# Performance work log

Measured on AMD Instinct MI355X. Metric: run time of the kernel, lower is better.

## Reference

```python
import jax, jax.numpy as jnp
import numpy as np

SOLVER_STEPS = 10
POINT_DIM = 2
CONTEXT_DIM = 128
HIDDEN_DIM = 256


def setup_inputs() -> dict:
    key = jax.random.key(0)
    ks = jax.random.split(key, 8)
    B, N = 64, 4096
    in_dim = POINT_DIM + 1 + CONTEXT_DIM  # 131
    std = 0.1  # torch nn.init.normal_(std=0.1)
    x = jax.random.normal(ks[0], (B, N, POINT_DIM), jnp.float32)
    context = jax.random.normal(ks[1], (B, CONTEXT_DIM), jnp.float32)
    w1 = std * jax.random.normal(ks[2], (in_dim, HIDDEN_DIM), jnp.float32)
    w2 = std * jax.random.normal(ks[3], (HIDDEN_DIM, HIDDEN_DIM), jnp.float32)
    w3 = std * jax.random.normal(ks[4], (HIDDEN_DIM, HIDDEN_DIM), jnp.float32)
    w4 = std * 0.1 * jax.random.normal(ks[5], (HIDDEN_DIM, POINT_DIM), jnp.float32)  # last layer weight * 0.1
    b1 = jnp.zeros((HIDDEN_DIM,), jnp.float32)
    b2 = jnp.zeros((HIDDEN_DIM,), jnp.float32)
    b3 = jnp.zeros((HIDDEN_DIM,), jnp.float32)
    b4 = jnp.zeros((POINT_DIM,), jnp.float32)
    return {"x": x, "context": context, "w1": w1, "b1": b1, "w2": w2, "b2": b2,
            "w3": w3, "b3": b3, "w4": w4, "b4": b4}


def _mlp(pts, t, ctx, w1, b1, w2, b2, w3, b3, w4, b4):
    # pts: [B,N,2], ctx: [B,N,C] -> velocity [B,N,2]
    B, N, _ = pts.shape
    t_vec = jnp.full((B, N, 1), t, dtype=pts.dtype)
    h = jnp.concatenate([pts, t_vec, ctx], axis=-1)
    h = jax.nn.silu(h @ w1 + b1)  # Swish == silu
    h = jax.nn.silu(h @ w2 + b2)
    h = jax.nn.silu(h @ w3 + b3)
    return h @ w4 + b4


def reference(x, context, w1, b1, w2, b2, w3, b3, w4, b4):
    B, N, D = x.shape
    ctx = jnp.broadcast_to(context[:, None, :], (B, N, context.shape[-1]))
    dt = jnp.asarray(1.0 / SOLVER_STEPS, x.dtype)
    ts = jnp.linspace(0.0, 1.0, SOLVER_STEPS + 1, dtype=x.dtype)[:SOLVER_STEPS]
    e0 = jnp.broadcast_to(jnp.array([1.0, 0.0], x.dtype), x.shape)
    e1 = jnp.broadcast_to(jnp.array([0.0, 1.0], x.dtype), x.shape)

    def step(carry, t_i):
        pts, log_det = carry
        f = lambda p: _mlp(p, t_i, ctx, w1, b1, w2, b2, w3, b3, w4, b4)
        # exact divergence = trace of per-point 2x2 Jacobian via two JVPs
        v, j0 = jax.jvp(f, (pts,), (e0,))
        _, j1 = jax.jvp(f, (pts,), (e1,))
        div = (j0[..., 0] + j1[..., 1])[..., None]  # [B,N,1]
        return (pts + v * dt, log_det + div * dt), None

    init = (x, jnp.zeros((B, N, 1), x.dtype))
    (final_pts, log_det), _ = jax.lax.scan(step, init, ts)
    final_log_det = log_det[..., 0].sum(axis=1, keepdims=True)  # [B,1]
    return final_pts, final_log_det
```

## Files before the change

### kernel.cpp

```cpp
#include <hip/hip_runtime.h>

typedef short bf16x8 __attribute__((ext_vector_type(8)));
typedef float f32x4 __attribute__((ext_vector_type(4)));
typedef float f32x16 __attribute__((ext_vector_type(16)));

#define AS 264
#define T0OFF (32 * AS)
#define T1OFF (64 * AS)

__device__ __forceinline__ unsigned short f2bf(float f) {
    union { float f; unsigned int u; } v; v.f = f;
    unsigned int u = v.u + 0x7FFFu + ((v.u >> 16) & 1u);
    return (unsigned short)(u >> 16);
}
__device__ __forceinline__ unsigned cvtpk(float a, float b) {
    unsigned r;
    asm("v_cvt_pk_bf16_f32 %0, %1, %2" : "=v"(r) : "v"(a), "v"(b));
    return r;
}
__device__ __forceinline__ float bf2f(unsigned int h) {
    union { unsigned int u; float f; } v; v.u = h << 16; return v.f;
}
__device__ __forceinline__ float sigm(float x) {
    return __builtin_amdgcn_rcpf(1.0f + __expf(-x));
}

struct f4s { float v[4]; };
__device__ __forceinline__ f4s ld4(const float* p) {
    float4 t = *(const float4*)p;
    f4s r; r.v[0] = t.x; r.v[1] = t.y; r.v[2] = t.z; r.v[3] = t.w; return r;
}


__global__ void k_base(const float* __restrict__ ctx,
                       const float* __restrict__ w1,
                       const float* __restrict__ b1,
                       float* __restrict__ base) {
    const int b = blockIdx.x, n = threadIdx.x;
    float acc = b1[n];
    for (int c = 0; c < 128; ++c)
        acc += ctx[b * 128 + c] * w1[(3 + c) * 256 + n];
    base[b * 256 + n] = acc;
}

__global__ void k_frag(const float* __restrict__ w,
                       unsigned short* __restrict__ wf) {
    const int t = blockIdx.x * blockDim.x + threadIdx.x;
    const int j = t & 7, lane = (t >> 3) & 63, hb = (t >> 9) & 7, kk = t >> 12;
    const int c = kk * 16 + (lane >> 5) * 8 + j;
    const int h = hb * 32 + (lane & 31);
    wf[t] = f2bf(w[c * 256 + h]);
}

#define MFMA6(koff, w0, w1)                                                        \
    {                                                                              \
        const bf16x8 fP  = *(const bf16x8*)(Asl + abase + (koff));                 \
        const bf16x8 fT0 = *(const bf16x8*)(Asl + abase + (koff) + T0OFF);         \
        const bf16x8 fT1 = *(const bf16x8*)(Asl + abase + (koff) + T1OFF);         \
        aP0  = __builtin_amdgcn_mfma_f32_32x32x16_bf16(w0, fP,  aP0,  0, 0, 0);    \
        aT00 = __builtin_amdgcn_mfma_f32_32x32x16_bf16(w0, fT0, aT00, 0, 0, 0);    \
        aT10 = __builtin_amdgcn_mfma_f32_32x32x16_bf16(w0, fT1, aT10, 0, 0, 0);    \
        aP1  = __builtin_amdgcn_mfma_f32_32x32x16_bf16(w1, fP,  aP1,  0, 0, 0);    \
        aT01 = __builtin_amdgcn_mfma_f32_32x32x16_bf16(w1, fT0, aT01, 0, 0, 0);    \
        aT11 = __builtin_amdgcn_mfma_f32_32x32x16_bf16(w1, fT1, aT11, 0, 0, 0);    \
    }

__device__ __forceinline__ void el_write32(unsigned short* Asl,
                                           const f32x16& aP, const f32x16& aT0, const f32x16& aT1,
                                           int ebase) {
#pragma unroll
    for (int g = 0; g < 4; ++g) {
        float h[4], t0[4], t1[4];
#pragma unroll
        for (int e = 0; e < 4; ++e) {
            const float pre = aP[4 * g + e];
            const float s = sigm(pre);
            const float hv = pre * s;
            const float dd = fmaf(hv, 1.0f - s, s);
            h[e]  = hv;
            t0[e] = dd * aT0[4 * g + e];
            t1[e] = dd * aT1[4 * g + e];
        }
        uint2 v0, v1, v2;
        v0.x = cvtpk(h[0],  h[1]);  v0.y = cvtpk(h[2],  h[3]);
        v1.x = cvtpk(t0[0], t0[1]); v1.y = cvtpk(t0[2], t0[3]);
        v2.x = cvtpk(t1[0], t1[1]); v2.y = cvtpk(t1[2], t1[3]);
        *(uint2*)(Asl + ebase + 8 * g)         = v0;
        *(uint2*)(Asl + ebase + 8 * g + T0OFF) = v1;
        *(uint2*)(Asl + ebase + 8 * g + T1OFF) = v2;
    }
}

__launch_bounds__(256, 2)
__global__ void k_main(const float* __restrict__ x,
                       const float* __restrict__ w1,
                       const float* __restrict__ b2g,
                       const float* __restrict__ b3g,
                       const float* __restrict__ w4g,
                       const float* __restrict__ b4g,
                       const unsigned short* __restrict__ w2f,
                       const unsigned short* __restrict__ w3f,
                       const float* __restrict__ basep,
                       float* __restrict__ ldacc,
                       float* __restrict__ out) {
    __shared__ unsigned short Asl[96 * AS];
    __shared__ float w1r[3][256];
    __shared__ float basel[256];
    __shared__ float w40[256], w41[256];
    __shared__ float b2l[256], b3l[256];
    __shared__ float px[32][2];
    __shared__ float pld[32];

    const int tid = threadIdx.x;
    const int wg = blockIdx.x;
    const int b = wg >> 7;
    const int n0 = (wg & 127) << 5;

    for (int i = tid; i < 768; i += 256) w1r[i >> 8][i & 255] = w1[i];
    {
        basel[tid] = basep[b * 256 + tid];
        w40[tid] = w4g[2 * tid]; w41[tid] = w4g[2 * tid + 1];
        b2l[tid] = b2g[tid];     b3l[tid] = b3g[tid];
    }
    if (tid < 64) ((float*)px)[tid] = x[((b << 12) + n0) * 2 + tid];
    if (tid < 32) pld[tid] = 0.0f;

    const int lane = tid & 63, wave = tid >> 6;
    const int p = lane & 31, kh = lane >> 5;
    const int hb0 = 2 * wave, hb1 = 2 * wave + 1;
    const int abase  = p * AS + kh * 8;
    const int ebase0 = p * AS + hb0 * 32 + kh * 4;
    const int ebase1 = p * AS + hb1 * 32 + kh * 4;
    const int wub0   = hb0 * 64 + lane;
    const int wub1   = hb1 * 64 + lane;
    const int bbase0 = hb0 * 32 + kh * 4;
    const int bbase1 = hb1 * 32 + kh * 4;

    const int p4 = tid >> 3;
    const int ic = tid & 7;

    const float b40 = b4g[0], b41 = b4g[1];
    __syncthreads();

#pragma unroll 1
    for (int st = 0; st < 10; ++st) {
        const float ti = 0.1f * (float)st;
        const float x0 = px[p4][0];
        const float x1 = px[p4][1];
#pragma unroll
        for (int g = 0; g < 8; ++g) {
            const int cb = g * 32 + (ic << 2);
            const f4s wa = ld4(&w1r[0][cb]);
            const f4s wb = ld4(&w1r[1][cb]);
            const f4s wc = ld4(&w1r[2][cb]);
            const f4s bs = ld4(&basel[cb]);
            float hf[4], t0f[4], t1f[4];
#pragma unroll
            for (int e = 0; e < 4; ++e) {
                const float pre = x0 * wa.v[e] + x1 * wb.v[e] + ti * wc.v[e] + bs.v[e];
                const float s = sigm(pre);
                const float h = pre * s;
                const float d = fmaf(h, 1.0f - s, s);
                hf[e]  = h;
                t0f[e] = d * wa.v[e];
                t1f[e] = d * wb.v[e];
            }
            uint2 v0, v1, v2;
            v0.x = cvtpk(hf[0],  hf[1]);  v0.y = cvtpk(hf[2],  hf[3]);
            v1.x = cvtpk(t0f[0], t0f[1]); v1.y = cvtpk(t0f[2], t0f[3]);
            v2.x = cvtpk(t1f[0], t1f[1]); v2.y = cvtpk(t1f[2], t1f[3]);
            *(uint2*)(Asl + p4 * AS + cb) = v0;
            *(uint2*)(Asl + T0OFF + p4 * AS + cb) = v1;
            *(uint2*)(Asl + T1OFF + p4 * AS + cb) = v2;
        }
        __syncthreads();

        f32x16 aP0, aT00, aT10, aP1, aT01, aT11;
#pragma unroll
        for (int g = 0; g < 4; ++g) {
            const float4 bv0 = *(const float4*)&b2l[bbase0 + 8 * g];
            const float4 bv1 = *(const float4*)&b2l[bbase1 + 8 * g];
            aP0[4 * g + 0] = bv0.x; aP0[4 * g + 1] = bv0.y;
            aP0[4 * g + 2] = bv0.z; aP0[4 * g + 3] = bv0.w;
            aP1[4 * g + 0] = bv1.x; aP1[4 * g + 1] = bv1.y;
            aP1[4 * g + 2] = bv1.z; aP1[4 * g + 3] = bv1.w;
        }
#pragma unroll
        for (int r = 0; r < 16; ++r) { aT00[r] = 0.f; aT10[r] = 0.f; aT01[r] = 0.f; aT11[r] = 0.f; }
        {
            const bf16x8* __restrict__ wp = (const bf16x8*)w2f;
            bf16x8 b0[4], b1[4];
#pragma unroll
            for (int i = 0; i < 4; ++i) { b0[i] = wp[wub0 + i * 512]; b1[i] = wp[wub1 + i * 512]; }
#pragma unroll 1
            for (int kk = 0; kk < 12; kk += 4) {
#pragma unroll
                for (int u = 0; u < 4; ++u) {
                    MFMA6((kk + u) * 16, b0[u], b1[u]);
                    b0[u] = wp[wub0 + (kk + 4 + u) * 512];
                    b1[u] = wp[wub1 + (kk + 4 + u) * 512];
                }
            }
#pragma unroll
            for (int u = 0; u < 4; ++u) MFMA6((12 + u) * 16, b0[u], b1[u]);
        }
        __syncthreads();
        el_write32(Asl, aP0, aT00, aT10, ebase0);
        el_write32(Asl, aP1, aT01, aT11, ebase1);
        __syncthreads();

#pragma unroll
        for (int g = 0; g < 4; ++g) {
            const float4 bv0 = *(const float4*)&b3l[bbase0 + 8 * g];
            const float4 bv1 = *(const float4*)&b3l[bbase1 + 8 * g];
            aP0[4 * g + 0] = bv0.x; aP0[4 * g + 1] = bv0.y;
            aP0[4 * g + 2] = bv0.z; aP0[4 * g + 3] = bv0.w;
            aP1[4 * g + 0] = bv1.x; aP1[4 * g + 1] = bv1.y;
            aP1[4 * g + 2] = bv1.z; aP1[4 * g + 3] = bv1.w;
        }
#pragma unroll
        for (int r = 0; r < 16; ++r) { aT00[r] = 0.f; aT10[r] = 0.f; aT01[r] = 0.f; aT11[r] = 0.f; }
        {
            const bf16x8* __restrict__ wp = (const bf16x8*)w3f;
            bf16x8 b0[4], b1[4];
#pragma unroll
            for (int i = 0; i < 4; ++i) { b0[i] = wp[wub0 + i * 512]; b1[i] = wp[wub1 + i * 512]; }
#pragma unroll 1
            for (int kk = 0; kk < 12; kk += 4) {
#pragma unroll
                for (int u = 0; u < 4; ++u) {
                    MFMA6((kk + u) * 16, b0[u], b1[u]);
                    b0[u] = wp[wub0 + (kk + 4 + u) * 512];
                    b1[u] = wp[wub1 + (kk + 4 + u) * 512];
                }
            }
#pragma unroll
            for (int u = 0; u < 4; ++u) MFMA6((12 + u) * 16, b0[u], b1[u]);
        }
        __syncthreads();
        el_write32(Asl, aP0, aT00, aT10, ebase0);
        el_write32(Asl, aP1, aT01, aT11, ebase1);
        __syncthreads();

        {
            float v0 = 0.f, v1 = 0.f, j00 = 0.f, j11 = 0.f;
#pragma unroll
            for (int g = 0; g < 8; ++g) {
                const int cb = g * 32 + (ic << 2);
                const uint2 hv  = *(const uint2*)(Asl + p4 * AS + cb);
                const uint2 t0v = *(const uint2*)(Asl + T0OFF + p4 * AS + cb);
                const uint2 t1v = *(const uint2*)(Asl + T1OFF + p4 * AS + cb);
                const f4s wa = ld4(&w40[cb]);
                const f4s wb = ld4(&w41[cb]);
                const unsigned hu[4]  = { hv.x & 0xffffu,  hv.x >> 16,  hv.y & 0xffffu,  hv.y >> 16 };
                const unsigned t0u[4] = { t0v.x & 0xffffu, t0v.x >> 16, t0v.y & 0xffffu, t0v.y >> 16 };
                const unsigned t1u[4] = { t1v.x & 0xffffu, t1v.x >> 16, t1v.y & 0xffffu, t1v.y >> 16 };
#pragma unroll
                for (int e = 0; e < 4; ++e) {
                    const float h = bf2f(hu[e]);
                    v0  += h * wa.v[e];
                    v1  += h * wb.v[e];
                    j00 += bf2f(t0u[e]) * wa.v[e];
                    j11 += bf2f(t1u[e]) * wb.v[e];
                }
            }
#pragma unroll
            for (int o = 1; o < 8; o <<= 1) {
                v0  += __shfl_xor(v0, o);
                v1  += __shfl_xor(v1, o);
                j00 += __shfl_xor(j00, o);
                j11 += __shfl_xor(j11, o);
            }
            if (ic == 0) {
                px[p4][0] += 0.1f * (v0 + b40);
                px[p4][1] += 0.1f * (v1 + b41);
                pld[p4]   += 0.1f * (j00 + j11);
            }
        }
    }

    if (ic == 0) {
        out[((b << 12) + n0 + p4) * 2]     = px[p4][0];
        out[((b << 12) + n0 + p4) * 2 + 1] = px[p4][1];
    }
    __syncthreads();
    if (wave == 0) {
        float v = (lane < 32) ? pld[lane] : 0.0f;
#pragma unroll
        for (int o = 32; o > 0; o >>= 1) v += __shfl_xor(v, o);
        if (lane == 0) atomicAdd(ldacc + b, v);
    }
}

__global__ void k_fin(const float* __restrict__ ldacc, float* __restrict__ out) {
    out[524288 + threadIdx.x] = ldacc[threadIdx.x];
}

extern "C" void kernel_launch(void* const* d_in, const int* in_sizes, int n_in,
                              void* d_out, int out_size, void* d_ws, size_t ws_size,
                              hipStream_t stream) {
    const float* x   = (const float*)d_in[0];
    const float* ctx = (const float*)d_in[1];
    const float* w1  = (const float*)d_in[2];
    const float* b1  = (const float*)d_in[3];
    const float* w2  = (const float*)d_in[4];
    const float* b2  = (const float*)d_in[5];
    const float* w3  = (const float*)d_in[6];
    const float* b3  = (const float*)d_in[7];
    const float* w4  = (const float*)d_in[8];
    const float* b4  = (const float*)d_in[9];

    char* ws = (char*)d_ws;
    unsigned short* w2f = (unsigned short*)ws;
    unsigned short* w3f = (unsigned short*)(ws + 131072);
    float* basep = (float*)(ws + 262144);
    float* ldacc = (float*)(ws + 327680);
    float* out = (float*)d_out;

    hipMemsetAsync(ldacc, 0, 64 * sizeof(float), stream);
    k_base<<<dim3(64), dim3(256), 0, stream>>>(ctx, w1, b1, basep);
    k_frag<<<dim3(128), dim3(512), 0, stream>>>(w2, w2f);
    k_frag<<<dim3(128), dim3(512), 0, stream>>>(w3, w3f);
    k_main<<<dim3(8192), dim3(256), 0, stream>>>(x, w1, b2, b3, w4, b4, w2f, w3f, basep, ldacc, out);
    k_fin<<<dim3(1), dim3(64), 0, stream>>>(ldacc, out);
}
```

Baseline: 2.236 ms.

## Fuse layer-3 activation and output projection into MFMA register epilogue

The layer-3 SiLU, its derivative and the final 256->2 projection (value plus the two Jacobian diagonal terms) are now computed directly on the MFMA accumulator registers. Previously the activations and tangents were written to shared memory as bf16 and reread. w4 is preloaded into per-thread registers, and partial sums are reduced through a small shared slab across the four waves. This removes an LDS round trip, a barrier and bf16 rounding in the last layer, at the cost of 64 extra registers per thread, which may hurt occupancy under the 2-block launch bound.

```diff
diff --git a/kernel.cpp b/kernel.cpp
--- a/kernel.cpp
+++ b/kernel.cpp
@@ -106,10 +106,9 @@
     __shared__ unsigned short Asl[96 * AS];
     __shared__ float w1r[3][256];
     __shared__ float basel[256];
-    __shared__ float w40[256], w41[256];
     __shared__ float b2l[256], b3l[256];
     __shared__ float px[32][2];
-    __shared__ float pld[32];
+    __shared__ float pslab[4][32][4];
 
     const int tid = threadIdx.x;
     const int wg = blockIdx.x;
@@ -117,13 +116,10 @@
     const int n0 = (wg & 127) << 5;
 
     for (int i = tid; i < 768; i += 256) w1r[i >> 8][i & 255] = w1[i];
-    {
-        basel[tid] = basep[b * 256 + tid];
-        w40[tid] = w4g[2 * tid]; w41[tid] = w4g[2 * tid + 1];
-        b2l[tid] = b2g[tid];     b3l[tid] = b3g[tid];
-    }
+    basel[tid] = basep[b * 256 + tid];
+    b2l[tid] = b2g[tid];
+    b3l[tid] = b3g[tid];
     if (tid < 64) ((float*)px)[tid] = x[((b << 12) + n0) * 2 + tid];
-    if (tid < 32) pld[tid] = 0.0f;
 
     const int lane = tid & 63, wave = tid >> 6;
     const int p = lane & 31, kh = lane >> 5;
@@ -139,7 +135,20 @@
     const int p4 = tid >> 3;
     const int ic = tid & 7;
 
+    float w4r0[32], w4r1[32];
+#pragma unroll
+    for (int hb = 0; hb < 2; ++hb)
+#pragma unroll
+        for (int g = 0; g < 4; ++g)
+#pragma unroll
+            for (int e = 0; e < 4; ++e) {
+                const int hidden = (2 * wave + hb) * 32 + kh * 4 + 8 * g + e;
+                w4r0[hb * 16 + g * 4 + e] = w4g[2 * hidden];
+                w4r1[hb * 16 + g * 4 + e] = w4g[2 * hidden + 1];
+            }
+
     const float b40 = b4g[0], b41 = b4g[1];
+    float pldreg = 0.0f;
     __syncthreads();
 
 #pragma unroll 1
@@ -237,58 +246,61 @@
 #pragma unroll
             for (int u = 0; u < 4; ++u) MFMA6((12 + u) * 16, b0[u], b1[u]);
         }
-        __syncthreads();
-        el_write32(Asl, aP0, aT00, aT10, ebase0);
-        el_write32(Asl, aP1, aT01, aT11, ebase1);
-        __syncthreads();
 
         {
-            float v0 = 0.f, v1 = 0.f, j00 = 0.f, j11 = 0.f;
-#pragma unroll
-            for (int g = 0; g < 8; ++g) {
-                const int cb = g * 32 + (ic << 2);
-                const uint2 hv  = *(const uint2*)(Asl + p4 * AS + cb);
-                const uint2 t0v = *(const uint2*)(Asl + T0OFF + p4 * AS + cb);
-                const uint2 t1v = *(const uint2*)(Asl + T1OFF + p4 * AS + cb);
-                const f4s wa = ld4(&w40[cb]);
-                const f4s wb = ld4(&w41[cb]);
-                const unsigned hu[4]  = { hv.x & 0xffffu,  hv.x >> 16,  hv.y & 0xffffu,  hv.y >> 16 };
-                const unsigned t0u[4] = { t0v.x & 0xffffu, t0v.x >> 16, t0v.y & 0xffffu, t0v.y >> 16 };
-                const unsigned t1u[4] = { t1v.x & 0xffffu, t1v.x >> 16, t1v.y & 0xffffu, t1v.y >> 16 };
-#pragma unroll
-                for (int e = 0; e < 4; ++e) {
-                    const float h = bf2f(hu[e]);
-                    v0  += h * wa.v[e];
-                    v1  += h * wb.v[e];
-                    j00 += bf2f(t0u[e]) * wa.v[e];
-                    j11 += bf2f(t1u[e]) * wb.v[e];
-                }
-            }
-#pragma unroll
-            for (int o = 1; o < 8; o <<= 1) {
-                v0  += __shfl_xor(v0, o);
-                v1  += __shfl_xor(v1, o);
-                j00 += __shfl_xor(j00, o);
-                j11 += __shfl_xor(j11, o);
-            }
-            if (ic == 0) {
-                px[p4][0] += 0.1f * (v0 + b40);
-                px[p4][1] += 0.1f * (v1 + b41);
-                pld[p4]   += 0.1f * (j00 + j11);
-            }
-        }
+            float v0p = 0.f, v1p = 0.f, j00p = 0.f, j11p = 0.f;
+#define EPI(AP, AT0, AT1, HB)                                                      \
+            _Pragma("unroll")                                                      \
+            for (int g = 0; g < 4; ++g) {                                          \
+                _Pragma("unroll")                                                  \
+                for (int e = 0; e < 4; ++e) {                                      \
+                    const float pre = AP[4 * g + e];                               \
+                    const float s = sigm(pre);                                     \
+                    const float hv = pre * s;                                      \
+                    const float dd = fmaf(hv, 1.0f - s, s);                        \
+                    const float wA = w4r0[(HB) * 16 + g * 4 + e];                  \
+                    const float wB = w4r1[(HB) * 16 + g * 4 + e];                  \
+                    v0p  = fmaf(hv, wA, v0p);                                      \
+                    v1p  = fmaf(hv, wB, v1p);                                      \
+                    j00p = fmaf(dd * AT0[4 * g + e], wA, j00p);                    \
+                    j11p = fmaf(dd * AT1[4 * g + e], wB, j11p);                    \
+                }                                                                  \
+            }
+            EPI(aP0, aT00, aT10, 0)
+            EPI(aP1, aT01, aT11, 1)
+#undef EPI
+            v0p  += __shfl_xor(v0p, 32);
+            v1p  += __shfl_xor(v1p, 32);
+            j00p += __shfl_xor(j00p, 32);
+            j11p += __shfl_xor(j11p, 32);
+            if (lane < 32) {
+                float4 t; t.x = v0p; t.y = v1p; t.z = j00p; t.w = j11p;
+                *(float4*)&pslab[wave][lane][0] = t;
+            }
+        }
+        __syncthreads();
+
+        if (tid < 32) {
+            const float4 a0 = *(const float4*)&pslab[0][tid][0];
+            const float4 a1 = *(const float4*)&pslab[1][tid][0];
+            const float4 a2 = *(const float4*)&pslab[2][tid][0];
+            const float4 a3 = *(const float4*)&pslab[3][tid][0];
+            const float v0 = a0.x + a1.x + a2.x + a3.x;
+            const float v1 = a0.y + a1.y + a2.y + a3.y;
+            const float dv = (a0.z + a1.z + a2.z + a3.z) + (a0.w + a1.w + a2.w + a3.w);
+            px[tid][0] += 0.1f * (v0 + b40);
+            px[tid][1] += 0.1f * (v1 + b41);
+            pldreg     += 0.1f * dv;
+        }
+        __syncthreads();
     }
 
-    if (ic == 0) {
-        out[((b << 12) + n0 + p4) * 2]     = px[p4][0];
-        out[((b << 12) + n0 + p4) * 2 + 1] = px[p4][1];
-    }
-    __syncthreads();
-    if (wave == 0) {
-        float v = (lane < 32) ? pld[lane] : 0.0f;
-#pragma unroll
-        for (int o = 32; o > 0; o >>= 1) v += __shfl_xor(v, o);
-        if (lane == 0) atomicAdd(ldacc + b, v);
+    if (tid < 32) {
+        float2 o; o.x = px[tid][0]; o.y = px[tid][1];
+        *(float2*)&out[((b << 12) + n0 + tid) * 2] = o;
+#pragma unroll
+        for (int o2 = 16; o2 > 0; o2 >>= 1) pldreg += __shfl_xor(pldreg, o2);
+        if (tid == 0) atomicAdd(ldacc + b, pldreg);
     }
 }
 
```

After: 2.397 ms. +7.2%, slower.
